# Performance work log

Measured on AMD Instinct MI355X. Metric: run time of the kernel, lower is better.

## Reference

```python
import jax, jax.numpy as jnp
import numpy as np


def setup_inputs() -> dict:
    key = jax.random.key(0)
    batch, n_tx, n_el, n_ax, n_ch = 1, 4, 128, 2048, 2
    Nz, Nx = 256, 256
    data = jax.random.normal(key, (batch, n_tx, n_el, n_ax, n_ch), dtype=jnp.float32)
    # Imaging grid: lateral x in [-19mm, 19mm], depth z in [5mm, 45mm]
    x = jnp.linspace(-0.019, 0.019, Nx, dtype=jnp.float32)
    z = jnp.linspace(0.005, 0.045, Nz, dtype=jnp.float32)
    zz, xx = jnp.meshgrid(z, x, indexing="ij")
    grid = jnp.stack([xx, jnp.zeros_like(xx), zz], axis=-1)  # (Nz, Nx, 3)
    # 128-element linear probe along x
    probe_x = jnp.linspace(-0.019, 0.019, n_el, dtype=jnp.float32)
    probe_geometry = jnp.stack([probe_x, jnp.zeros(n_el, jnp.float32), jnp.zeros(n_el, jnp.float32)], axis=-1)
    t0_delays = jnp.zeros((n_tx, n_el), jnp.float32)   # plane wave at 0 deg per tx
    initial_times = jnp.zeros((n_tx,), jnp.float32)
    fs = jnp.float32(25e6)
    sound_speed = jnp.float32(1540.0)
    fc = jnp.float32(6.25e6)
    fdemod = jnp.float32(6.25e6)
    f_number = jnp.float32(1.0)
    return dict(data=data, grid=grid, probe_geometry=probe_geometry,
                initial_times=initial_times, t0_delays=t0_delays,
                fs=fs, sound_speed=sound_speed, fc=fc, fdemod=fdemod, f_number=f_number)


def reference(data, grid, probe_geometry, initial_times, t0_delays,
              fs, sound_speed, fc, fdemod, f_number):
    batch, n_tx, n_el, n_ax, n_ch = data.shape
    Nz, Nx, _ = grid.shape
    flatgrid = grid.reshape(-1, 3)                         # (P, 3)
    P = flatgrid.shape[0]

    # --- delays ---
    diff = flatgrid[None, :, :] - probe_geometry[:, None, :]   # (n_el, P, 3)
    el_dist = jnp.sqrt(jnp.sum(diff * diff, axis=-1))          # (n_el, P)
    # generic tx distance: min over elements of t0*c + |pix - el|
    tx_dist = jnp.min(t0_delays[:, :, None] * sound_speed + el_dist[None], axis=1)  # (n_tx, P)
    txdel = (tx_dist / sound_speed - initial_times[:, None]) * fs   # (n_tx, P) samples
    rxdel = el_dist / sound_speed * fs                              # (n_el, P) samples

    # --- f-number apodization mask (n_el, P) ---
    aperture = flatgrid[:, 2] / f_number
    lateral = jnp.abs(flatgrid[None, :, 0] - probe_geometry[:, None, 0])
    mask = (lateral <= aperture[None, :] / 2).astype(data.dtype)

    # --- fractional-delay gather + linear interpolation ---
    delays = txdel[:, None, :] + rxdel[None, :, :]          # (n_tx, n_el, P)
    d0 = jnp.clip(jnp.floor(delays).astype(jnp.int32), 0, n_ax - 1)
    d1 = jnp.clip(d0 + 1, 0, n_ax - 1)
    idx_shape = (batch, n_tx, n_el, P, n_ch)
    iq0 = jnp.take_along_axis(data, jnp.broadcast_to(d0[None, :, :, :, None], idx_shape), axis=3)
    iq1 = jnp.take_along_axis(data, jnp.broadcast_to(d1[None, :, :, :, None], idx_shape), axis=3)
    d0f = d0.astype(delays.dtype)
    d1f = d1.astype(delays.dtype)
    w0 = (d1f - delays)[None, :, :, :, None]
    w1 = (delays - d0f)[None, :, :, :, None]
    tof = (w0 * iq0 + w1 * iq1) * mask[None, None, :, :, None]  # (batch, n_tx, n_el, P, n_ch)

    # --- complex phase rotation (IQ demodulated data) ---
    if n_ch == 2:
        tshift = delays / fs                              # (n_tx, n_el, P)
        tdemod = flatgrid[:, 2] * 2 / sound_speed          # (P,)
        theta = 2 * jnp.pi * fc * (tshift - tdemod[None, None, :])
        ct = jnp.cos(theta)[None]
        st = jnp.sin(theta)[None]
        i, q = tof[..., 0], tof[..., 1]
        tof = jnp.stack([i * ct - q * st, q * ct + i * st], axis=-1)

    # (batch, n_tx, n_el, P, n_ch) -> (batch, n_tx, Nz, Nx, n_el, n_ch)
    out = jnp.transpose(tof, (0, 1, 3, 2, 4)).reshape(batch, n_tx, Nz, Nx, n_el, n_ch)
    return out
```

## Files before the change

kernel.cpp:

```cpp
#include <hip/hip_runtime.h>

#define BLOCK 256
#define PIX   16
#define ESUB  16
#define PIXG  32
#define ESUBG 8

typedef float f32x4 __attribute__((ext_vector_type(4)));
typedef float f32x2 __attribute__((ext_vector_type(2)));

__device__ __forceinline__ void decode_bid(int bid, int nx, int n_tx, int swz,
                                           int& tx, int& pblk, int& b) {
    if (swz) {
        const int g   = 8 / n_tx;
        const int xcd = bid & 7;
        const int s   = bid >> 3;
        tx = xcd % n_tx;
        const int idx = s * g + (xcd / n_tx);
        pblk = idx % nx;
        b    = idx / nx;
    } else {
        pblk = bid % nx;
        tx   = (bid / nx) % n_tx;
        b    = bid / (nx * n_tx);
    }
}

__global__ __launch_bounds__(BLOCK) void bf128(
    const float* __restrict__ data,
    const float* __restrict__ grd,
    const float* __restrict__ probe,
    const float* __restrict__ itimes,
    const float* __restrict__ t0,
    const float* __restrict__ fs_p, const float* __restrict__ c_p,
    const float* __restrict__ fc_p, const float* __restrict__ fn_p,
    int n_tx, int n_ax, int P, int nx, int swz,
    float2* __restrict__ out)
{
    constexpr int NEL = 128, NPASS = 8;
    __shared__ __align__(16) float2 tile[PIX][NEL];
    __shared__ float smin[ESUB][PIX];

    int tx, pblk, b;
    decode_bid(blockIdx.x, nx, n_tx, swz, tx, pblk, b);
    const int txb = b * n_tx + tx;

    const int t    = threadIdx.x;
    const int pix  = t & (PIX - 1);
    const int esub = t >> 4;
    const int p0   = pblk * PIX;
    const int p    = p0 + pix;

    const float fs  = *fs_p;
    const float c   = *c_p;
    const float fcv = *fc_p;
    const float fn  = *fn_p;

    const float px = grd[3 * p + 0];
    const float pz = grd[3 * p + 2];

    float dxr[NPASS], eldr[NPASS];
    {
        const float* __restrict__ t0row = t0 + tx * NEL;
        float mn = 3.4e38f;
#pragma unroll
        for (int k = 0; k < NPASS; ++k) {
            const int el = k * ESUB + esub;
            const float dx = px - probe[3 * el];
            const float eld = sqrtf(dx * dx + pz * pz);
            dxr[k] = dx;
            eldr[k] = eld;
            mn = fminf(mn, t0row[el] * c + eld);
        }
        smin[esub][pix] = mn;
    }
    const float it_tx = itimes[tx];
    __syncthreads();
    float m2 = smin[0][pix];
#pragma unroll
    for (int k = 1; k < ESUB; ++k) m2 = fminf(m2, smin[k][pix]);
    const float txd = (m2 / c - it_tx) * fs;

    const float half_ap   = (pz / fn) * 0.5f;
    const float fs_over_c = fs / c;
    const float ka        = fcv / fs;
    const float revb      = fcv * (2.0f * pz / c);

    const float2* __restrict__ dat =
        (const float2*)data + (size_t)txb * NEL * n_ax;

#if __has_builtin(__builtin_amdgcn_sinf) && __has_builtin(__builtin_amdgcn_cosf)
#define BF_SINCOS(r, s, cc) do { (s) = __builtin_amdgcn_sinf(r);            \
                                 (cc) = __builtin_amdgcn_cosf(r); } while (0)
#else
#define BF_SINCOS(r, s, cc) __sincosf((r) * 6.28318530717958647692f, &(s), &(cc))
#endif

#define BF_BODY(K0, K1)                                                     \
    _Pragma("unroll")                                                       \
    for (int k = (K0); k < (K1); ++k) {                                     \
        const int el = k * ESUB + esub;                                     \
        const float dx = dxr[k];                                            \
        const float m  = (fabsf(dx) <= half_ap) ? 1.0f : 0.0f;              \
        float2 res = make_float2(0.0f, 0.0f);                               \
        if (__ballot(m != 0.0f) != 0ull) {                                  \
            if (m != 0.0f) {                                                \
                const float del = fmaf(eldr[k], fs_over_c, txd);            \
                int i0 = (int)floorf(del);                                  \
                i0 = min(max(i0, 0), n_ax - 1);                             \
                const int i1 = min(i0 + 1, n_ax - 1);                       \
                const float w1 = del - (float)i0;                           \
                const float w0 = (float)i1 - del;                           \
                const float2 sA = dat[el * n_ax + i0];                      \
                const float2 sB = dat[el * n_ax + i1];                      \
                const float vi = w0 * sA.x + w1 * sB.x;                     \
                const float vq = w0 * sA.y + w1 * sB.y;                     \
                float rev = fmaf(del, ka, -revb);                           \
                rev -= floorf(rev);                                         \
                float st, ct;                                               \
                BF_SINCOS(rev, st, ct);                                     \
                res = make_float2(vi * ct - vq * st, vq * ct + vi * st);    \
            }                                                               \
        }                                                                   \
        tile[pix][el ^ (pix << 1)] = res;                                   \
    }

    const f32x4* __restrict__ t4 = (const f32x4*)&tile[0][0];
    f32x4* __restrict__ o4 = (f32x4*)(out + ((size_t)txb * P + p0) * NEL);

    const int spp = t >> 4;
    const int sj0 = t & 15;

#define BF_QUARTER(Q)                                                       \
    BF_BODY(2 * (Q), 2 * (Q) + 2)                                           \
    __syncthreads();                                                        \
    {                                                                       \
        const int jj = (Q) * 16 + sj0;                                      \
        __builtin_nontemporal_store(t4[spp * 64 + (jj ^ spp)],              \
                                    &o4[spp * 64 + jj]);                    \
    }

    BF_QUARTER(0)
    BF_QUARTER(1)
    BF_QUARTER(2)
    BF_QUARTER(3)
#undef BF_QUARTER
#undef BF_BODY
#undef BF_SINCOS
}

__global__ __launch_bounds__(BLOCK) void bf_tiled(
    const float* __restrict__ data, const float* __restrict__ grd,
    const float* __restrict__ probe, const float* __restrict__ itimes,
    const float* __restrict__ t0,
    const float* __restrict__ fs_p, const float* __restrict__ c_p,
    const float* __restrict__ fc_p, const float* __restrict__ fn_p,
    int n_tx, int n_el, int n_ax, int P, int nx, int swz,
    float2* __restrict__ out)
{
    __shared__ __align__(16) float2 tile[PIXG][128];
    __shared__ float smin[ESUBG][PIXG];
    __shared__ float txd_s[PIXG];

    int tx, pblk, b;
    decode_bid(blockIdx.x, nx, n_tx, swz, tx, pblk, b);
    const int txb = b * n_tx + tx;

    const int t    = threadIdx.x;
    const int pix  = t & (PIXG - 1);
    const int esub = t >> 5;
    const int p0   = pblk * PIXG;
    const int p    = p0 + pix;

    const float fs  = *fs_p;
    const float c   = *c_p;
    const float fcv = *fc_p;
    const float fn  = *fn_p;

    const float px = grd[3 * p + 0];
    const float pz = grd[3 * p + 2];

    const int npass = n_el / ESUBG;
    {
        float mn = 3.4e38f;
        for (int k = 0; k < npass; ++k) {
            const int el = k * ESUBG + esub;
            const float dx = px - probe[3 * el];
            mn = fminf(mn, t0[tx * n_el + el] * c + sqrtf(dx * dx + pz * pz));
        }
        smin[esub][pix] = mn;
    }
    __syncthreads();
    if (t < PIXG) {
        float m2 = smin[0][t];
#pragma unroll
        for (int k = 1; k < ESUBG; ++k) m2 = fminf(m2, smin[k][t]);
        txd_s[t] = (m2 / c - itimes[tx]) * fs;
    }
    __syncthreads();

    const float txd       = txd_s[pix];
    const float half_ap   = (pz / fn) * 0.5f;
    const float fs_over_c = fs / c;
    const float twopifc   = 6.28318530717958647692f * fcv;
    const float th_a      = twopifc / fs;
    const float th_b      = twopifc * (2.0f * pz / c);

    const float2* __restrict__ dat =
        (const float2*)data + (size_t)txb * n_el * n_ax;

    for (int k = 0; k < npass; ++k) {
        const int el = k * ESUBG + esub;
        const float dx = px - probe[3 * el];
        const float m  = (fabsf(dx) <= half_ap) ? 1.0f : 0.0f;
        float2 res = make_float2(0.0f, 0.0f);
        if (__ballot(m != 0.0f) != 0ull) {
            if (m != 0.0f) {
                const float eld = sqrtf(dx * dx + pz * pz);
                const float del = fmaf(eld, fs_over_c, txd);
                int i0 = (int)floorf(del);
                i0 = min(max(i0, 0), n_ax - 1);
                const int i1 = min(i0 + 1, n_ax - 1);
                const float w1 = del - (float)i0;
                const float w0 = (float)i1 - del;
                const float2 sA = dat[(size_t)el * n_ax + i0];
                const float2 sB = dat[(size_t)el * n_ax + i1];
                const float vi = w0 * sA.x + w1 * sB.x;
                const float vq = w0 * sA.y + w1 * sB.y;
                float st, ct;
                __sincosf(fmaf(del, th_a, -th_b), &st, &ct);
                res = make_float2(vi * ct - vq * st, vq * ct + vi * st);
            }
        }
        tile[pix][el ^ ((pix & 15) << 1)] = res;
    }
    __syncthreads();

    float2* __restrict__ op = out + ((size_t)txb * P + p0) * n_el;
    f32x2* __restrict__ o2 = (f32x2*)op;
    const f32x2* __restrict__ t2 = (const f32x2*)&tile[0][0];
    for (int f = t; f < PIXG * n_el; f += BLOCK) {
        const int pp = f / n_el;
        const int ee = f - pp * n_el;
        __builtin_nontemporal_store(t2[pp * 128 + (ee ^ ((pp & 15) << 1))], &o2[f]);
    }
}

extern "C" void kernel_launch(void* const* d_in, const int* in_sizes, int n_in,
                              void* d_out, int out_size, void* d_ws, size_t ws_size,
                              hipStream_t stream) {
    (void)d_ws; (void)ws_size;
    const float* data   = (const float*)d_in[0];
    const float* grd    = (const float*)d_in[1];
    const float* probe  = (const float*)d_in[2];
    const float* itimes = (const float*)d_in[3];
    const float* t0     = (const float*)d_in[4];
    const float* fs_p   = (const float*)d_in[5];
    const float* c_p    = (const float*)d_in[6];
    const float* fc_p   = (const float*)d_in[7];
    const float* fn_p   = (const float*)d_in[9];

    const int P    = in_sizes[1] / 3;
    const int n_el = in_sizes[2] / 3;
    const int n_tx = in_sizes[3];
    const long long batch =
        (long long)out_size / ((long long)n_tx * P * n_el * 2);
    const int n_ax =
        (int)(in_sizes[0] / (batch * (long long)n_tx * n_el * 2));

    if (n_el == 128 && P % PIX == 0) {
        const int nx   = P / PIX;
        const int nblk = nx * n_tx * (int)batch;
        const int swz  = (n_tx > 0 && 8 % n_tx == 0 && nblk % 8 == 0) ? 1 : 0;
        hipLaunchKernelGGL(bf128, dim3(nblk), dim3(BLOCK), 0, stream,
                           data, grd, probe, itimes, t0,
                           fs_p, c_p, fc_p, fn_p,
                           n_tx, n_ax, P, nx, swz, (float2*)d_out);
    } else {
        const int nx   = P / PIXG;
        const int nblk = nx * n_tx * (int)batch;
        const int swz  = (n_tx > 0 && 8 % n_tx == 0 && nblk % 8 == 0) ? 1 : 0;
        hipLaunchKernelGGL(bf_tiled, dim3(nblk), dim3(BLOCK), 0, stream,
                           data, grd, probe, itimes, t0,
                           fs_p, c_p, fc_p, fn_p,
                           n_tx, n_el, n_ax, P, nx, swz, (float2*)d_out);
    }
}
```

Baseline: 60.20 us.

## Cut register use in bf128: recompute distances, halve barriers, raise occupancy hint

Stops caching per-element dx and distance arrays in registers and recomputes them inside the main loop instead. It also sets launch bounds to 8 blocks per CU, splits the tile store into two halves (two barriers instead of four, the second a raw s_barrier after an LDS waitcnt), and hoists the row offset for data addressing. The aim is higher occupancy and fewer syncs, paid for with extra sqrt and probe loads per element. The second barrier relies on the manual lgkmcnt wait for correctness.

Result: slower. 68.70 us (+14.1%).

```diff
diff --git a/kernel.cpp b/kernel.cpp
--- a/kernel.cpp
+++ b/kernel.cpp
@@ -26,7 +26,19 @@
     }
 }
 
-__global__ __launch_bounds__(BLOCK) void bf128(
+__device__ __forceinline__ void barrier_lgkm() {
+    asm volatile("s_waitcnt lgkmcnt(0)" ::: "memory");
+    __builtin_amdgcn_s_barrier();
+}
+
+#if __has_builtin(__builtin_amdgcn_sinf) && __has_builtin(__builtin_amdgcn_cosf)
+#define BF_SINCOS(r, s, cc) do { (s) = __builtin_amdgcn_sinf(r);            \
+                                 (cc) = __builtin_amdgcn_cosf(r); } while (0)
+#else
+#define BF_SINCOS(r, s, cc) __sincosf((r) * 6.28318530717958647692f, &(s), &(cc))
+#endif
+
+__global__ __launch_bounds__(BLOCK, 8) void bf128(
     const float* __restrict__ data,
     const float* __restrict__ grd,
     const float* __restrict__ probe,
@@ -37,7 +49,7 @@
     int n_tx, int n_ax, int P, int nx, int swz,
     float2* __restrict__ out)
 {
-    constexpr int NEL = 128, NPASS = 8;
+    constexpr int NEL = 128, NPASS = 8, HALFP = 4;
     __shared__ __align__(16) float2 tile[PIX][NEL];
     __shared__ float smin[ESUB][PIX];
 
@@ -56,10 +68,10 @@
     const float fcv = *fc_p;
     const float fn  = *fn_p;
 
-    const float px = grd[3 * p + 0];
-    const float pz = grd[3 * p + 2];
-
-    float dxr[NPASS], eldr[NPASS];
+    const float px  = grd[3 * p + 0];
+    const float pz  = grd[3 * p + 2];
+    const float pz2 = pz * pz;
+
     {
         const float* __restrict__ t0row = t0 + tx * NEL;
         float mn = 3.4e38f;
@@ -67,10 +79,7 @@
         for (int k = 0; k < NPASS; ++k) {
             const int el = k * ESUB + esub;
             const float dx = px - probe[3 * el];
-            const float eld = sqrtf(dx * dx + pz * pz);
-            dxr[k] = dx;
-            eldr[k] = eld;
-            mn = fminf(mn, t0row[el] * c + eld);
+            mn = fminf(mn, t0row[el] * c + sqrtf(dx * dx + pz2));
         }
         smin[esub][pix] = mn;
     }
@@ -88,31 +97,27 @@
 
     const float2* __restrict__ dat =
         (const float2*)data + (size_t)txb * NEL * n_ax;
-
-#if __has_builtin(__builtin_amdgcn_sinf) && __has_builtin(__builtin_amdgcn_cosf)
-#define BF_SINCOS(r, s, cc) do { (s) = __builtin_amdgcn_sinf(r);            \
-                                 (cc) = __builtin_amdgcn_cosf(r); } while (0)
-#else
-#define BF_SINCOS(r, s, cc) __sincosf((r) * 6.28318530717958647692f, &(s), &(cc))
-#endif
+    const int row_off = esub * n_ax;
 
 #define BF_BODY(K0, K1)                                                     \
     _Pragma("unroll")                                                       \
     for (int k = (K0); k < (K1); ++k) {                                     \
         const int el = k * ESUB + esub;                                     \
-        const float dx = dxr[k];                                            \
+        const float dx = px - probe[3 * el];                                \
         const float m  = (fabsf(dx) <= half_ap) ? 1.0f : 0.0f;              \
         float2 res = make_float2(0.0f, 0.0f);                               \
         if (__ballot(m != 0.0f) != 0ull) {                                  \
             if (m != 0.0f) {                                                \
-                const float del = fmaf(eldr[k], fs_over_c, txd);            \
+                const float eld = sqrtf(dx * dx + pz2);                     \
+                const float del = fmaf(eld, fs_over_c, txd);                \
                 int i0 = (int)floorf(del);                                  \
                 i0 = min(max(i0, 0), n_ax - 1);                             \
                 const int i1 = min(i0 + 1, n_ax - 1);                       \
                 const float w1 = del - (float)i0;                           \
                 const float w0 = (float)i1 - del;                           \
-                const float2 sA = dat[el * n_ax + i0];                      \
-                const float2 sB = dat[el * n_ax + i1];                      \
+                const float2* __restrict__ rowp = dat + k * ESUB * n_ax;    \
+                const float2 sA = rowp[row_off + i0];                       \
+                const float2 sB = rowp[row_off + i1];                       \
                 const float vi = w0 * sA.x + w1 * sB.x;                     \
                 const float vq = w0 * sA.y + w1 * sB.y;                     \
                 float rev = fmaf(del, ka, -revb);                           \
@@ -131,22 +136,23 @@
     const int spp = t >> 4;
     const int sj0 = t & 15;
 
-#define BF_QUARTER(Q)                                                       \
-    BF_BODY(2 * (Q), 2 * (Q) + 2)                                           \
-    __syncthreads();                                                        \
-    {                                                                       \
-        const int jj = (Q) * 16 + sj0;                                      \
-        __builtin_nontemporal_store(t4[spp * 64 + (jj ^ spp)],              \
-                                    &o4[spp * 64 + jj]);                    \
-    }
-
-    BF_QUARTER(0)
-    BF_QUARTER(1)
-    BF_QUARTER(2)
-    BF_QUARTER(3)
-#undef BF_QUARTER
+    BF_BODY(0, HALFP)
+    __syncthreads();
+#pragma unroll
+    for (int h = 0; h < 2; ++h) {
+        const int jj = h * 16 + sj0;
+        __builtin_nontemporal_store(t4[spp * 64 + (jj ^ spp)],
+                                    &o4[spp * 64 + jj]);
+    }
+    BF_BODY(HALFP, NPASS)
+    barrier_lgkm();
+#pragma unroll
+    for (int h = 0; h < 2; ++h) {
+        const int jj = 32 + h * 16 + sj0;
+        __builtin_nontemporal_store(t4[spp * 64 + (jj ^ spp)],
+                                    &o4[spp * 64 + jj]);
+    }
 #undef BF_BODY
-#undef BF_SINCOS
 }
 
 __global__ __launch_bounds__(BLOCK) void bf_tiled(
```
